# Kernel tuning notes

Hardware: AMD Instinct MI355X
Metric: run time of the kernel (lower is better)

The kernel has to match this reference:

```python
import jax, jax.numpy as jnp
import numpy as np

K = 5            # srn kernel size (kernels[0])
EPSILON = 1e-3   # epsilons -> SRN additive noise scale
BN_EPS = 1e-5
NUM_SLICES = 3
OUT_CH = 64
CLASSES = 5


def _unfold(x, k):
    # torch.nn.Unfold, padding=0: (B, C*k*k, L), channel-major then (kh, kw) row-major
    B, C, H, W = x.shape
    Ho, Wo = H - k + 1, W - k + 1
    cols = jnp.stack([x[:, :, i:i + Ho, j:j + Wo]
                      for i in range(k) for j in range(k)], axis=2)  # (B,C,k*k,Ho,Wo)
    return cols.reshape(B, C * k * k, Ho * Wo), Ho, Wo


def _bn(x, g, b):
    # BatchNorm2d in training mode: batch statistics, biased variance
    m = x.mean((0, 2, 3), keepdims=True)
    v = x.var((0, 2, 3), keepdims=True)
    return (x - m) * jax.lax.rsqrt(v + BN_EPS) * g[None, :, None, None] + b[None, :, None, None]


def _conv(x, w, b):
    y = jax.lax.conv_general_dilated(x, w, (1, 1), 'VALID',
                                     dimension_numbers=('NCHW', 'OIHW', 'NCHW'))
    return y + b[None, :, None, None]


def _avgpool(x, s):
    B, C, H, W = x.shape
    return x.reshape(B, C, H // s, s, W // s, s).mean((3, 5))


def _maxpool(x, s):
    B, C, H, W = x.shape
    return x.reshape(B, C, H // s, s, W // s, s).max((3, 5))


def _srn(x, srn_w):
    B = x.shape[0]
    y, Ho, Wo = _unfold(x, K)                               # (B, n, L)
    y = y + EPSILON * jax.random.normal(jax.random.key(42), y.shape, y.dtype)
    gg = jnp.std(y, axis=1, ddof=1, keepdims=True)          # torch.std is unbiased
    y = y / gg
    O, C, _, _, S = srn_w.shape
    n = C * K * K
    X = srn_w.reshape(O, n, S)
    X = jnp.concatenate([jnp.ones((O, n, 1), X.dtype), X], axis=2)   # (O, n, S+1)
    Xcov = jnp.einsum('onf,ong->ofg', X, X)                 # X^T X, (O, 4, 4)
    Xinv = jnp.linalg.inv(Xcov)
    M = jnp.einsum('ofg,ong->ofn', Xinv, X)
    Wc = jnp.einsum('ofn,bnl->bofl', M, y)
    pred = jnp.einsum('onf,bofl->bonl', X, Wc)              # fitted values (B,O,n,L)
    err = jnp.mean((y[:, None] - pred) ** 2, axis=2)        # (B,O,L)
    err = err.reshape(B, O, Ho, Wo)
    A = (jnp.exp(-err) - np.exp(-1.0)) / (1.0 - np.exp(-1.0))
    return A - 0.5


def setup_inputs() -> dict:
    key = jax.random.key(0)
    ks = jax.random.split(key, 12)
    x = jax.random.normal(ks[0], (4, 3, 64, 64), jnp.float32)
    # xavier-style init scaled up for numerical stability of the small-matrix inverse
    srn_w = 0.05 * jax.random.normal(ks[1], (OUT_CH, 3, K, K, NUM_SLICES), jnp.float32)
    conv2_w = 0.05 * jax.random.normal(ks[2], (128, 64, 3, 3), jnp.float32)
    conv2_b = 0.01 * jax.random.normal(ks[3], (128,), jnp.float32)
    conv3_w = 0.05 * jax.random.normal(ks[4], (128, 128, 3, 3), jnp.float32)
    conv3_b = 0.01 * jax.random.normal(ks[5], (128,), jnp.float32)
    conv4_w = 0.05 * jax.random.normal(ks[6], (128, 128, 3, 3), jnp.float32)
    conv4_b = 0.01 * jax.random.normal(ks[7], (128,), jnp.float32)
    bn1_g = jnp.ones((64,), jnp.float32); bn1_b = jnp.zeros((64,), jnp.float32)
    bn2_g = jnp.ones((128,), jnp.float32); bn2_b = jnp.zeros((128,), jnp.float32)
    bn3_g = jnp.ones((128,), jnp.float32); bn3_b = jnp.zeros((128,), jnp.float32)
    bn4_g = jnp.ones((128,), jnp.float32); bn4_b = jnp.zeros((128,), jnp.float32)
    fc2_w = 0.05 * jax.random.normal(ks[8], (CLASSES, 128, 1, 1), jnp.float32)
    fc2_b = 0.01 * jax.random.normal(ks[9], (CLASSES,), jnp.float32)
    return dict(x=x, srn_w=srn_w, conv2_w=conv2_w, conv2_b=conv2_b,
                conv3_w=conv3_w, conv3_b=conv3_b, conv4_w=conv4_w, conv4_b=conv4_b,
                bn1_g=bn1_g, bn1_b=bn1_b, bn2_g=bn2_g, bn2_b=bn2_b,
                bn3_g=bn3_g, bn3_b=bn3_b, bn4_g=bn4_g, bn4_b=bn4_b,
                fc2_w=fc2_w, fc2_b=fc2_b)


def reference(x, srn_w, conv2_w, conv2_b, conv3_w, conv3_b, conv4_w, conv4_b,
              bn1_g, bn1_b, bn2_g, bn2_b, bn3_g, bn3_b, bn4_g, bn4_b,
              fc2_w, fc2_b):
    h = _srn(x, srn_w)                                      # (B,64,60,60)
    h = _avgpool(h, 2)
    h = _bn(h, bn1_g, bn1_b)
    h = jax.nn.relu(_bn(_conv(h, conv2_w, conv2_b), bn2_g, bn2_b))
    h = _avgpool(h, 2)
    h = jax.nn.relu(_bn(_conv(h, conv3_w, conv3_b), bn3_g, bn3_b))
    h = _maxpool(h, 2)
    h = jax.nn.relu(_bn(_conv(h, conv4_w, conv4_b), bn4_g, bn4_b))
    h = _maxpool(h, 4)                                      # (B,128,1,1)
    flat = h.reshape(h.shape[0], -1)                        # (B,128)
    return flat @ fc2_w.reshape(CLASSES, -1).T + fc2_b      # 1x1 conv == matmul
```

## Files before the change

### kernel.cpp

```cpp
#include <hip/hip_runtime.h>
#include <math.h>

__device__ __align__(16) float g_w2p[9 * 2304 * 4];
__device__ __align__(16) float g_w3p[17 * 2304 * 4];
__device__ __align__(16) float g_w4p[8 * 4608 * 4];
__device__ __align__(16) float g_h1[4 * 30 * 30 * 64];
__device__ __align__(16) float g_h2[4 * 14 * 14 * 4 * 128];
__device__ __align__(16) float g_h3[4 * 6 * 6 * 4 * 128];
__device__ __align__(16) float g_h4[4 * 16 * 128];

__global__ __launch_bounds__(256) void k_srn(const float* __restrict__ x,
                                             const float* __restrict__ srn_w,
                                             const float* __restrict__ w2,
                                             float* __restrict__ stats) {
    __shared__ __align__(16) float wlds[64 * 244];
    __shared__ float xsm[648];
    __shared__ float part[2 * 15 * 66];
    __shared__ float redS[256], redQ[256];
    int bid = blockIdx.x, t = threadIdx.x;
    int b = bid / 60, rem = bid % 60, r = rem >> 1, ch = rem & 1;

    for (int j = bid * 256 + t; j < 73728; j += 240 * 256) {
        int c = j & 3, s4 = j >> 2;
        int sl = s4 % 36, tmp = s4 / 36, oc_l = tmp & 63, blk = tmp >> 6;
        int it = blk & 3, ocg = blk >> 2;
        int kw = sl % 3, icq = (sl / 3) & 3, kh = sl / 12;
        int ic = it * 16 + icq * 4 + c;
        g_w2p[j] = w2[((ocg * 64 + oc_l) * 64 + ic) * 9 + kh * 3 + kw];
    }

    float4 wr[15];
#pragma unroll
    for (int k = 0; k < 15; k++) {
        int i4 = k * 256 + t;
        if (i4 < 3600) wr[k] = ((const float4*)srn_w)[i4];
    }
    float xr[3];
#pragma unroll
    for (int k = 0; k < 3; k++) {
        int i = t + k * 256;
        if (i < 648) {
            int c = i / 216, rm = i % 216, rr = rm / 36, col = rm % 36;
            int gc = ch * 30 + col; if (gc > 63) gc = 63;
            xr[k] = x[((b * 3 + c) * 64 + (2 * r + rr)) * 64 + gc];
        }
    }
#pragma unroll
    for (int k = 0; k < 15; k++) {
        int i4 = k * 256 + t;
        if (i4 < 3600) {
            float v[4] = { wr[k].x, wr[k].y, wr[k].z, wr[k].w };
#pragma unroll
            for (int e = 0; e < 4; e++) {
                int i = i4 * 4 + e, o = i / 225, j = i % 225;
                wlds[o * 244 + (j / 15) * 16 + (j % 15)] = v[e];
            }
        }
    }
#pragma unroll
    for (int k = 0; k < 3; k++) { int i = t + k * 256; if (i < 648) xsm[i] = xr[k]; }
    __syncthreads();

    int w = t >> 6, o = t & 63;
    int rw = w & 1, cq = w >> 1, base = cq * 16;

    float z1[16], z2[16], z3[16], s[16], q[16];
#pragma unroll
    for (int i = 0; i < 16; i++) { z1[i]=0; z2[i]=0; z3[i]=0; s[i]=0; q[i]=0; }

    for (int c = 0; c < 3; c++) {
#pragma unroll
        for (int kh = 0; kh < 5; kh++) {
            float xv[20];
#pragma unroll
            for (int k = 0; k < 20; k++) xv[k] = xsm[(c * 6 + rw + kh) * 36 + base + k];
            float wf[16];
            const float* wp = &wlds[o * 244 + (c * 5 + kh) * 16];
            *(float4*)&wf[0]  = *(const float4*)&wp[0];
            *(float4*)&wf[4]  = *(const float4*)&wp[4];
            *(float4*)&wf[8]  = *(const float4*)&wp[8];
            *(float4*)&wf[12] = *(const float4*)&wp[12];
#pragma unroll
            for (int kw = 0; kw < 5; kw++) {
                float w1 = wf[kw * 3], w2v = wf[kw * 3 + 1], w3v = wf[kw * 3 + 2];
#pragma unroll
                for (int i = 0; i < 16; i++) {
                    float v = xv[kw + i];
                    s[i] += v; q[i] += v * v;
                    z1[i] += w1 * v; z2[i] += w2v * v; z3[i] += w3v * v;
                }
            }
        }
    }

    float gm[16];
    {
        float c01=0,c02=0,c03=0,c11=0,c12=0,c13=0,c22=0,c23=0,c33=0;
#pragma unroll
        for (int row = 0; row < 15; row++) {
            float wf[16];
            const float* wp = &wlds[o * 244 + row * 16];
            *(float4*)&wf[0]  = *(const float4*)&wp[0];
            *(float4*)&wf[4]  = *(const float4*)&wp[4];
            *(float4*)&wf[8]  = *(const float4*)&wp[8];
            *(float4*)&wf[12] = *(const float4*)&wp[12];
#pragma unroll
            for (int kw = 0; kw < 5; kw++) {
                float w1 = wf[kw*3], w2v = wf[kw*3+1], w3v = wf[kw*3+2];
                c01 += w1; c02 += w2v; c03 += w3v;
                c11 += w1*w1; c12 += w1*w2v; c13 += w1*w3v;
                c22 += w2v*w2v; c23 += w2v*w3v; c33 += w3v*w3v;
            }
        }
        float A[4][8];
        A[0][0]=75.f; A[0][1]=c01; A[0][2]=c02; A[0][3]=c03;
        A[1][0]=c01;  A[1][1]=c11; A[1][2]=c12; A[1][3]=c13;
        A[2][0]=c02;  A[2][1]=c12; A[2][2]=c22; A[2][3]=c23;
        A[3][0]=c03;  A[3][1]=c13; A[3][2]=c23; A[3][3]=c33;
#pragma unroll
        for (int i = 0; i < 4; i++)
#pragma unroll
            for (int j = 0; j < 4; j++) A[i][4 + j] = (i == j) ? 1.f : 0.f;
#pragma unroll
        for (int p = 0; p < 4; p++) {
            float ip = 1.f / A[p][p];
#pragma unroll
            for (int j = 0; j < 8; j++) A[p][j] *= ip;
#pragma unroll
            for (int i = 0; i < 4; i++) if (i != p) {
                float f = A[i][p];
#pragma unroll
                for (int j = 0; j < 8; j++) A[i][j] -= f * A[p][j];
            }
        }
#pragma unroll
        for (int i = 0; i < 4; i++)
#pragma unroll
            for (int j = 0; j < 4; j++) gm[i * 4 + j] = A[i][4 + j];
    }

    const float C1 = 0.36787944117144233f;
    const float INV = 1.5819767068693265f;
#pragma unroll
    for (int pp = 0; pp < 8; pp++) {
        int pl = cq * 8 + pp;
        if (pl < 15) {
            float aa = 0.f;
#pragma unroll
            for (int e = 0; e < 2; e++) {
                int i = 2 * pp + e;
                float sum = s[i], sq = q[i];
                float gg2 = (sq - sum * sum * (1.f / 75.f)) * (1.f / 74.f);
                float zf[4] = { sum, z1[i], z2[i], z3[i] };
                float qf = 0.f;
#pragma unroll
                for (int f = 0; f < 4; f++) {
                    float acc = 0.f;
#pragma unroll
                    for (int h = 0; h < 4; h++) acc += gm[f * 4 + h] * zf[h];
                    qf += acc * zf[f];
                }
                float err = (sq - qf) / (75.f * gg2);
                aa += (expf(-err) - C1) * INV - 0.5f;
            }
            part[(rw * 15 + pl) * 66 + o] = 0.25f * aa;
        }
    }
    __syncthreads();

    int j = t >> 6;
    float ps = 0.f, pq = 0.f;
    for (int pl = j; pl < 15; pl += 4) {
        float v = part[pl * 66 + o] + part[(15 + pl) * 66 + o];
        g_h1[((b * 30 + r) * 30 + ch * 15 + pl) * 64 + o] = v;
        ps += v; pq += v * v;
    }
    redS[t] = ps; redQ[t] = pq;
    __syncthreads();
    if (t < 64) {
        atomicAdd(&stats[t],      redS[t] + redS[64 + t] + redS[128 + t] + redS[192 + t]);
        atomicAdd(&stats[64 + t], redQ[t] + redQ[64 + t] + redQ[128 + t] + redQ[192 + t]);
    }
}

__global__ __launch_bounds__(256) void k_conv2(const float* __restrict__ w3,
                                               const float* __restrict__ g1,
                                               const float* __restrict__ b1,
                                               float* __restrict__ stats) {
    __shared__ __align__(16) float ws[64 * 148];
    __shared__ __align__(16) float xs[3 * 30 * 64];
    __shared__ float redS[256], redQ[256];
    int blk = blockIdx.x;
    int b = blk / 56, rem = blk % 56, oh = rem >> 1, ocg = rem & 1;
    int t = threadIdx.x;
    int oc_l = t & 63, qtr = t >> 6, owb = qtr * 7;

    for (int j = blk * 256 + t; j < 147456; j += 224 * 256) {
        int c = j & 3, s4 = j >> 2;
        int sl = s4 % 36, tmp = s4 / 36, oc2 = tmp & 63, bk = tmp >> 6;
        int it = bk & 7, og = bk >> 3;
        int kw = sl % 3, icq = (sl / 3) & 3, kh = sl / 12;
        int ic = it * 16 + icq * 4 + c;
        g_w3p[j] = w3[((og * 64 + oc2) * 128 + ic) * 9 + kh * 3 + kw];
    }

    {
        int icb = (t & 15) * 4;
        float4 S = *(const float4*)&stats[icb], Q = *(const float4*)&stats[64 + icb];
        float4 G4 = *(const float4*)&g1[icb], B4 = *(const float4*)&b1[icb];
        float scv[4], shv[4];
        float mm[4] = { S.x, S.y, S.z, S.w }, qq[4] = { Q.x, Q.y, Q.z, Q.w };
        float gg[4] = { G4.x, G4.y, G4.z, G4.w }, bb[4] = { B4.x, B4.y, B4.z, B4.w };
#pragma unroll
        for (int c = 0; c < 4; c++) {
            float m = mm[c] * (1.f / 3600.f);
            float v = qq[c] * (1.f / 3600.f) - m * m;
            scv[c] = gg[c] * rsqrtf(v + 1e-5f);
            shv[c] = bb[c] - m * scv[c];
        }
        const float4* src4 = (const float4*)(g_h1 + (b * 900 + oh * 30) * 64);
        float4 xr[6];
#pragma unroll
        for (int k = 0; k < 6; k++) { int i4 = t + k * 256; if (i4 < 1440) xr[k] = src4[i4]; }
        const float4* wsrc0 = (const float4*)g_w2p;
        float4 wreg[9];
#pragma unroll
        for (int k = 0; k < 9; k++) wreg[k] = wsrc0[(ocg * 4) * 2304 + k * 256 + t];
#pragma unroll
        for (int k = 0; k < 6; k++) {
            int i4 = t + k * 256;
            if (i4 < 1440) {
                float4 v;
                v.x = xr[k].x * scv[0] + shv[0]; v.y = xr[k].y * scv[1] + shv[1];
                v.z = xr[k].z * scv[2] + shv[2]; v.w = xr[k].w * scv[3] + shv[3];
                *(float4*)&xs[i4 * 4] = v;
            }
        }
#pragma unroll
        for (int k = 0; k < 9; k++) {
            int idx = k * 256 + t;
            *(float4*)&ws[(idx / 36) * 148 + (idx % 36) * 4] = wreg[k];
        }
    }
    __syncthreads();

    float acc[7] = {0, 0, 0, 0, 0, 0, 0};
    const float4* wsrc = (const float4*)g_w2p + (ocg * 4) * 2304;
    for (int it = 0; it < 4; ++it) {
        float4 wreg[9];
        if (it < 3) {
#pragma unroll
            for (int k = 0; k < 9; k++) wreg[k] = wsrc[(it + 1) * 2304 + k * 256 + t];
        }
#pragma unroll 1
        for (int icq = 0; icq < 4; icq++) {
            int xoff = it * 16 + icq * 4;
#pragma unroll
            for (int kh = 0; kh < 3; kh++) {
                const float* wb = &ws[oc_l * 148 + (kh * 4 + icq) * 12];
                float4 w0 = *(const float4*)&wb[0];
                float4 w1 = *(const float4*)&wb[4];
                float4 w2v = *(const float4*)&wb[8];
                const float* xrow = &xs[(kh * 30 + owb) * 64 + xoff];
                float4 x0 = *(const float4*)&xrow[0];
                float4 x1 = *(const float4*)&xrow[64];
#pragma unroll
                for (int i = 0; i < 7; i++) {
                    float4 x2 = *(const float4*)&xrow[(i + 2) * 64];
                    acc[i] += w0.x * x0.x + w0.y * x0.y + w0.z * x0.z + w0.w * x0.w
                            + w1.x * x1.x + w1.y * x1.y + w1.z * x1.z + w1.w * x1.w
                            + w2v.x * x2.x + w2v.y * x2.y + w2v.z * x2.z + w2v.w * x2.w;
                    x0 = x1; x1 = x2;
                }
            }
        }
        if (it < 3) {
            __syncthreads();
#pragma unroll
            for (int k = 0; k < 9; k++) {
                int idx = k * 256 + t;
                *(float4*)&ws[(idx / 36) * 148 + (idx % 36) * 4] = wreg[k];
            }
            __syncthreads();
        }
    }
    int oc = ocg * 64 + oc_l;
    float ps = 0.f, pq = 0.f;
#pragma unroll
    for (int i = 0; i < 7; i++) {
        int ow = owb + i;
        g_h2[(((b * 14 + (oh >> 1)) * 14 + (ow >> 1)) * 4 + (oh & 1) * 2 + (ow & 1)) * 128 + oc] = acc[i];
        ps += acc[i]; pq += acc[i] * acc[i];
    }
    redS[t] = ps; redQ[t] = pq;
    __syncthreads();
    if (t < 64) {
        atomicAdd(&stats[128 + ocg * 64 + t], redS[t] + redS[64 + t] + redS[128 + t] + redS[192 + t]);
        atomicAdd(&stats[256 + ocg * 64 + t], redQ[t] + redQ[64 + t] + redQ[128 + t] + redQ[192 + t]);
    }
}

__global__ __launch_bounds__(256) void k_conv3(const float* __restrict__ w4,
                                               const float* __restrict__ g2,
                                               const float* __restrict__ b2,
                                               float* __restrict__ stats) {
    __shared__ __align__(16) float ws[64 * 148];
    __shared__ __align__(16) float xs[3 * 14 * 128];
    __shared__ float redS[256], redQ[256];
    int blk = blockIdx.x;
    int b = blk / 24, rem = blk % 24, oh = rem >> 1, ocg = rem & 1;
    int t = threadIdx.x;
    int oc_l = t & 63, qtr = t >> 6, owb = qtr * 3;

    for (int j = blk * 256 + t; j < 147456; j += 96 * 256) {
        int c = j & 3, s4 = j >> 2;
        int sl = s4 % 72, tmp = s4 / 72, oc2 = tmp & 15, blkq = tmp >> 4;
        int icq = blkq & 3, og = blkq >> 2;
        int kw = sl % 3, icb2 = (sl / 3) & 7, kh = sl / 24;
        int ic = icq * 32 + icb2 * 4 + c;
        g_w4p[j] = w4[((og * 16 + oc2) * 128 + ic) * 9 + kh * 3 + kw];
    }

    {
        int icb = (t & 31) * 4;
        float4 S = *(const float4*)&stats[128 + icb], Q = *(const float4*)&stats[256 + icb];
        float4 G4 = *(const float4*)&g2[icb], B4 = *(const float4*)&b2[icb];
        float scv[4], shv[4];
        float mm[4] = { S.x, S.y, S.z, S.w }, qq[4] = { Q.x, Q.y, Q.z, Q.w };
        float gg[4] = { G4.x, G4.y, G4.z, G4.w }, bb[4] = { B4.x, B4.y, B4.z, B4.w };
#pragma unroll
        for (int c = 0; c < 4; c++) {
            float m = mm[c] * (1.f / 3136.f);
            float v = qq[c] * (1.f / 3136.f) - m * m;
            scv[c] = gg[c] * rsqrtf(v + 1e-5f);
            shv[c] = bb[c] - m * scv[c];
        }
        const float4* wsrc0 = (const float4*)g_w3p;
        float4 wreg[9];
#pragma unroll
        for (int k = 0; k < 9; k++) wreg[k] = wsrc0[(ocg * 8) * 2304 + k * 256 + t];
        float4 pa[6], pb[6], pc[6], pd[6];
#pragma unroll
        for (int k = 0; k < 6; k++) {
            int i4 = t + k * 256;
            if (i4 < 1344) {
                int px = (i4 >> 5) % 14, rr = i4 / 448;
                const float4* p0 = (const float4*)&g_h2[(((b * 14 + oh + rr) * 14 + px) * 4) * 128 + (i4 & 31) * 4];
                pa[k] = p0[0]; pb[k] = p0[32]; pc[k] = p0[64]; pd[k] = p0[96];
            }
        }
#pragma unroll
        for (int k = 0; k < 9; k++) {
            int idx = k * 256 + t;
            *(float4*)&ws[(idx / 36) * 148 + (idx % 36) * 4] = wreg[k];
        }
#pragma unroll
        for (int k = 0; k < 6; k++) {
            int i4 = t + k * 256;
            if (i4 < 1344) {
                float4 o4;
                o4.x = 0.25f * (fmaxf(pa[k].x * scv[0] + shv[0], 0.f) + fmaxf(pb[k].x * scv[0] + shv[0], 0.f)
                              + fmaxf(pc[k].x * scv[0] + shv[0], 0.f) + fmaxf(pd[k].x * scv[0] + shv[0], 0.f));
                o4.y = 0.25f * (fmaxf(pa[k].y * scv[1] + shv[1], 0.f) + fmaxf(pb[k].y * scv[1] + shv[1], 0.f)
                              + fmaxf(pc[k].y * scv[1] + shv[1], 0.f) + fmaxf(pd[k].y * scv[1] + shv[1], 0.f));
                o4.z = 0.25f * (fmaxf(pa[k].z * scv[2] + shv[2], 0.f) + fmaxf(pb[k].z * scv[2] + shv[2], 0.f)
                              + fmaxf(pc[k].z * scv[2] + shv[2], 0.f) + fmaxf(pd[k].z * scv[2] + shv[2], 0.f));
                o4.w = 0.25f * (fmaxf(pa[k].w * scv[3] + shv[3], 0.f) + fmaxf(pb[k].w * scv[3] + shv[3], 0.f)
                              + fmaxf(pc[k].w * scv[3] + shv[3], 0.f) + fmaxf(pd[k].w * scv[3] + shv[3], 0.f));
                *(float4*)&xs[i4 * 4] = o4;
            }
        }
    }
    __syncthreads();

    float acc[3] = {0, 0, 0};
    const float4* wsrc = (const float4*)g_w3p + (ocg * 8) * 2304;
    for (int it = 0; it < 8; ++it) {
        float4 wreg[9];
        if (it < 7) {
#pragma unroll
            for (int k = 0; k < 9; k++) wreg[k] = wsrc[(it + 1) * 2304 + k * 256 + t];
        }
#pragma unroll 1
        for (int icq = 0; icq < 4; icq++) {
            int xoff = it * 16 + icq * 4;
#pragma unroll
            for (int kh = 0; kh < 3; kh++) {
                const float* wb = &ws[oc_l * 148 + (kh * 4 + icq) * 12];
                float4 w0 = *(const float4*)&wb[0];
                float4 w1 = *(const float4*)&wb[4];
                float4 w2v = *(const float4*)&wb[8];
                const float* xrow = &xs[(kh * 14 + owb) * 128 + xoff];
                float4 x0 = *(const float4*)&xrow[0];
                float4 x1 = *(const float4*)&xrow[128];
#pragma unroll
                for (int i = 0; i < 3; i++) {
                    float4 x2 = *(const float4*)&xrow[(i + 2) * 128];
                    acc[i] += w0.x * x0.x + w0.y * x0.y + w0.z * x0.z + w0.w * x0.w
                            + w1.x * x1.x + w1.y * x1.y + w1.z * x1.z + w1.w * x1.w
                            + w2v.x * x2.x + w2v.y * x2.y + w2v.z * x2.z + w2v.w * x2.w;
                    x0 = x1; x1 = x2;
                }
            }
        }
        if (it < 7) {
            __syncthreads();
#pragma unroll
            for (int k = 0; k < 9; k++) {
                int idx = k * 256 + t;
                *(float4*)&ws[(idx / 36) * 148 + (idx % 36) * 4] = wreg[k];
            }
            __syncthreads();
        }
    }
    int oc = ocg * 64 + oc_l;
    float ps = 0.f, pq = 0.f;
#pragma unroll
    for (int i = 0; i < 3; i++) {
        int ow = owb + i;
        g_h3[(((b * 6 + (oh >> 1)) * 6 + (ow >> 1)) * 4 + (oh & 1) * 2 + (ow & 1)) * 128 + oc] = acc[i];
        ps += acc[i]; pq += acc[i] * acc[i];
    }
    redS[t] = ps; redQ[t] = pq;
    __syncthreads();
    if (t < 64) {
        atomicAdd(&stats[384 + ocg * 64 + t], redS[t] + redS[64 + t] + redS[128 + t] + redS[192 + t]);
        atomicAdd(&stats[512 + ocg * 64 + t], redQ[t] + redQ[64 + t] + redQ[128 + t] + redQ[192 + t]);
    }
}

__global__ __launch_bounds__(256) void k_conv4(const float* __restrict__ g3,
                                               const float* __restrict__ b3,
                                               float* __restrict__ stats) {
    __shared__ __align__(16) float ws[64 * 292];
    __shared__ __align__(16) float xs[3 * 6 * 128];
    __shared__ float red[256];
    int blk = blockIdx.x;
    int b = blk / 32, rem = blk % 32, oh = rem / 8, ocg = rem % 8;
    int t = threadIdx.x;
    int oc_l = t & 15, ow = (t >> 4) & 3, icq = t >> 6;

    {
        int icb = (t & 31) * 4;
        float4 S = *(const float4*)&stats[384 + icb], Q = *(const float4*)&stats[512 + icb];
        float4 G4 = *(const float4*)&g3[icb], B4 = *(const float4*)&b3[icb];
        float scv[4], shv[4];
        float mm[4] = { S.x, S.y, S.z, S.w }, qq[4] = { Q.x, Q.y, Q.z, Q.w };
        float gg[4] = { G4.x, G4.y, G4.z, G4.w }, bb[4] = { B4.x, B4.y, B4.z, B4.w };
#pragma unroll
        for (int c = 0; c < 4; c++) {
            float m = mm[c] * (1.f / 576.f);
            float v = qq[c] * (1.f / 576.f) - m * m;
            scv[c] = gg[c] * rsqrtf(v + 1e-5f);
            shv[c] = bb[c] - m * scv[c];
        }
        const float4* wsrc = (const float4*)g_w4p + ocg * 4608;
        float4 wreg[18];
#pragma unroll
        for (int k = 0; k < 18; k++) wreg[k] = wsrc[k * 256 + t];
        float4 pa[3], pb[3], pc[3], pd[3];
#pragma unroll
        for (int k = 0; k < 3; k++) {
            int i4 = t + k * 256;
            if (i4 < 576) {
                int px = (i4 >> 5) % 6, rr = i4 / 192;
                const float4* p0 = (const float4*)&g_h3[(((b * 6 + oh + rr) * 6 + px) * 4) * 128 + (i4 & 31) * 4];
                pa[k] = p0[0]; pb[k] = p0[32]; pc[k] = p0[64]; pd[k] = p0[96];
            }
        }
#pragma unroll
        for (int k = 0; k < 18; k++) {
            int idx = k * 256 + t;
            *(float4*)&ws[(idx / 72) * 292 + (idx % 72) * 4] = wreg[k];
        }
#pragma unroll
        for (int k = 0; k < 3; k++) {
            int i4 = t + k * 256;
            if (i4 < 576) {
                float4 o4;
                o4.x = fmaxf(fmaxf(fmaxf(pa[k].x * scv[0] + shv[0], pb[k].x * scv[0] + shv[0]),
                                   fmaxf(pc[k].x * scv[0] + shv[0], pd[k].x * scv[0] + shv[0])), 0.f);
                o4.y = fmaxf(fmaxf(fmaxf(pa[k].y * scv[1] + shv[1], pb[k].y * scv[1] + shv[1]),
                                   fmaxf(pc[k].y * scv[1] + shv[1], pd[k].y * scv[1] + shv[1])), 0.f);
                o4.z = fmaxf(fmaxf(fmaxf(pa[k].z * scv[2] + shv[2], pb[k].z * scv[2] + shv[2]),
                                   fmaxf(pc[k].z * scv[2] + shv[2], pd[k].z * scv[2] + shv[2])), 0.f);
                o4.w = fmaxf(fmaxf(fmaxf(pa[k].w * scv[3] + shv[3], pb[k].w * scv[3] + shv[3]),
                                   fmaxf(pc[k].w * scv[3] + shv[3], pd[k].w * scv[3] + shv[3])), 0.f);
                *(float4*)&xs[i4 * 4] = o4;
            }
        }
    }
    __syncthreads();

    float acc = 0.f;
    const float* wbase = &ws[(icq * 16 + oc_l) * 292];
#pragma unroll 1
    for (int icbq = 0; icbq < 8; icbq++) {
#pragma unroll
        for (int kh = 0; kh < 3; kh++) {
            const float* wb = &wbase[(kh * 8 + icbq) * 12];
            float4 w0 = *(const float4*)&wb[0];
            float4 w1 = *(const float4*)&wb[4];
            float4 w2v = *(const float4*)&wb[8];
            float4 x0 = *(const float4*)&xs[(kh * 6 + ow) * 128 + icq * 32 + icbq * 4];
            float4 x1 = *(const float4*)&xs[(kh * 6 + ow + 1) * 128 + icq * 32 + icbq * 4];
            float4 x2 = *(const float4*)&xs[(kh * 6 + ow + 2) * 128 + icq * 32 + icbq * 4];
            acc += w0.x * x0.x + w0.y * x0.y + w0.z * x0.z + w0.w * x0.w
                 + w1.x * x1.x + w1.y * x1.y + w1.z * x1.z + w1.w * x1.w
                 + w2v.x * x2.x + w2v.y * x2.y + w2v.z * x2.z + w2v.w * x2.w;
        }
    }
    red[t] = acc;
    __syncthreads();
    if (t < 64) {
        float v = red[t] + red[t + 64] + red[t + 128] + red[t + 192];
        int oc = ocg * 16 + (t & 15);
        g_h4[((b * 4 + oh) * 4 + (t >> 4)) * 128 + oc] = v;
        float ps = v + __shfl_xor(v, 16);  ps += __shfl_xor(ps, 32);
        float pv = v * v;
        float pq = pv + __shfl_xor(pv, 16); pq += __shfl_xor(pq, 32);
        if (t < 16) {
            atomicAdd(&stats[640 + ocg * 16 + t], ps);
            atomicAdd(&stats[768 + ocg * 16 + t], pq);
        }
    }
}

__global__ __launch_bounds__(256) void k_final(const float* __restrict__ g4,
                                               const float* __restrict__ b4,
                                               const float* __restrict__ fcw,
                                               const float* __restrict__ fcb,
                                               const float* __restrict__ stats,
                                               float* __restrict__ out) {
    __shared__ float sc[128], sh[128];
    __shared__ float pooled[4][128];
    int t = threadIdx.x;
    if (t < 128) {
        float m = stats[640 + t] * (1.f / 64.f);
        float v = stats[768 + t] * (1.f / 64.f) - m * m;
        float rs = rsqrtf(v + 1e-5f);
        sc[t] = g4[t] * rs; sh[t] = b4[t] - m * sc[t];
    }
    __syncthreads();
    for (int item = t; item < 512; item += 256) {
        int b = item >> 7, oc = item & 127;
        float s = sc[oc], h = sh[oc];
        float mx = 0.f;
#pragma unroll
        for (int k = 0; k < 16; k++) mx = fmaxf(mx, g_h4[(b * 16 + k) * 128 + oc] * s + h);
        pooled[b][oc] = mx;
    }
    __syncthreads();
    if (t < 20) {
        int b = t / 5, cls = t % 5;
        float acc = fcb[cls];
        const float* w = &fcw[cls * 128];
        for (int oc = 0; oc < 128; oc++) acc += pooled[b][oc] * w[oc];
        out[b * 5 + cls] = acc;
    }
}

extern "C" void kernel_launch(void* const* d_in, const int* in_sizes, int n_in,
                              void* d_out, int out_size, void* d_ws, size_t ws_size,
                              hipStream_t stream) {
    (void)in_sizes; (void)n_in; (void)out_size; (void)ws_size;
    const float* x     = (const float*)d_in[0];
    const float* srn_w = (const float*)d_in[1];
    const float* w2    = (const float*)d_in[2];
    const float* w3    = (const float*)d_in[4];
    const float* w4    = (const float*)d_in[6];
    const float* g1 = (const float*)d_in[8];  const float* b1 = (const float*)d_in[9];
    const float* g2 = (const float*)d_in[10]; const float* b2 = (const float*)d_in[11];
    const float* g3 = (const float*)d_in[12]; const float* b3 = (const float*)d_in[13];
    const float* g4 = (const float*)d_in[14]; const float* b4 = (const float*)d_in[15];
    const float* fcw = (const float*)d_in[16]; const float* fcb = (const float*)d_in[17];
    float* out = (float*)d_out;
    float* stats = (float*)d_ws;

    hipMemsetAsync(d_ws, 0, 4096, stream);
    k_srn  <<<dim3(240), dim3(256), 0, stream>>>(x, srn_w, w2, stats);
    k_conv2<<<dim3(224), dim3(256), 0, stream>>>(w3, g1, b1, stats);
    k_conv3<<<dim3(96),  dim3(256), 0, stream>>>(w4, g2, b2, stats);
    k_conv4<<<dim3(128), dim3(256), 0, stream>>>(g3, b3, stats);
    k_final<<<dim3(1),   dim3(256), 0, stream>>>(g4, b4, fcw, fcb, stats, out);
}
```

Baseline: 111.2 us.

## Double parallelism in SRN/conv kernels and replace stat atomics with per-block partials

Result: slower. 144.6 us (+30.1%).

```diff
diff --git a/kernel.cpp b/kernel.cpp
--- a/kernel.cpp
+++ b/kernel.cpp
@@ -1,44 +1,53 @@
 #include <hip/hip_runtime.h>
 #include <math.h>
 
-__device__ __align__(16) float g_w2p[9 * 2304 * 4];
-__device__ __align__(16) float g_w3p[17 * 2304 * 4];
+#define P1S 0
+#define P1Q 15360
+#define P2S 30720
+#define P2Q 45056
+#define P3S 59392
+#define P3Q 65536
+#define P4S 71680
+#define P4Q 73728
+
+__device__ __align__(16) float g_w2p[16 * 1152 * 4];
+__device__ __align__(16) float g_w3p[32 * 1152 * 4];
 __device__ __align__(16) float g_w4p[8 * 4608 * 4];
 __device__ __align__(16) float g_h1[4 * 30 * 30 * 64];
 __device__ __align__(16) float g_h2[4 * 14 * 14 * 4 * 128];
 __device__ __align__(16) float g_h3[4 * 6 * 6 * 4 * 128];
 __device__ __align__(16) float g_h4[4 * 16 * 128];
 
-__global__ __launch_bounds__(256) void k_srn(const float* __restrict__ x,
+__global__ __launch_bounds__(512) void k_srn(const float* __restrict__ x,
                                              const float* __restrict__ srn_w,
                                              const float* __restrict__ w2,
-                                             float* __restrict__ stats) {
+                                             float* __restrict__ ws) {
     __shared__ __align__(16) float wlds[64 * 244];
     __shared__ float xsm[648];
     __shared__ float part[2 * 15 * 66];
-    __shared__ float redS[256], redQ[256];
+    __shared__ float redS[512], redQ[512];
     int bid = blockIdx.x, t = threadIdx.x;
     int b = bid / 60, rem = bid % 60, r = rem >> 1, ch = rem & 1;
 
-    for (int j = bid * 256 + t; j < 73728; j += 240 * 256) {
+    for (int j = bid * 512 + t; j < 73728; j += 240 * 512) {
         int c = j & 3, s4 = j >> 2;
-        int sl = s4 % 36, tmp = s4 / 36, oc_l = tmp & 63, blk = tmp >> 6;
+        int sl = s4 % 36, tmp = s4 / 36, oc_l = tmp & 31, blk = tmp >> 5;
         int it = blk & 3, ocg = blk >> 2;
         int kw = sl % 3, icq = (sl / 3) & 3, kh = sl / 12;
         int ic = it * 16 + icq * 4 + c;
-        g_w2p[j] = w2[((ocg * 64 + oc_l) * 64 + ic) * 9 + kh * 3 + kw];
-    }
-
-    float4 wr[15];
-#pragma unroll
-    for (int k = 0; k < 15; k++) {
-        int i4 = k * 256 + t;
+        g_w2p[j] = w2[((ocg * 32 + oc_l) * 64 + ic) * 9 + kh * 3 + kw];
+    }
+
+    float4 wr[8];
+#pragma unroll
+    for (int k = 0; k < 8; k++) {
+        int i4 = k * 512 + t;
         if (i4 < 3600) wr[k] = ((const float4*)srn_w)[i4];
     }
-    float xr[3];
-#pragma unroll
-    for (int k = 0; k < 3; k++) {
-        int i = t + k * 256;
+    float xr[2];
+#pragma unroll
+    for (int k = 0; k < 2; k++) {
+        int i = k * 512 + t;
         if (i < 648) {
             int c = i / 216, rm = i % 216, rr = rm / 36, col = rm % 36;
             int gc = ch * 30 + col; if (gc > 63) gc = 63;
@@ -46,34 +55,34 @@
         }
     }
 #pragma unroll
-    for (int k = 0; k < 15; k++) {
-        int i4 = k * 256 + t;
+    for (int k = 0; k < 8; k++) {
+        int i4 = k * 512 + t;
         if (i4 < 3600) {
-            float v[4] = { wr[k].x, wr[k].y, wr[k].z, wr[k].w };
+            float v4[4] = { wr[k].x, wr[k].y, wr[k].z, wr[k].w };
 #pragma unroll
             for (int e = 0; e < 4; e++) {
-                int i = i4 * 4 + e, o = i / 225, j = i % 225;
-                wlds[o * 244 + (j / 15) * 16 + (j % 15)] = v[e];
-            }
-        }
-    }
-#pragma unroll
-    for (int k = 0; k < 3; k++) { int i = t + k * 256; if (i < 648) xsm[i] = xr[k]; }
+                int i = i4 * 4 + e, o = i / 225, jj = i % 225;
+                wlds[o * 244 + (jj / 15) * 16 + (jj % 15)] = v4[e];
+            }
+        }
+    }
+#pragma unroll
+    for (int k = 0; k < 2; k++) { int i = k * 512 + t; if (i < 648) xsm[i] = xr[k]; }
     __syncthreads();
 
     int w = t >> 6, o = t & 63;
-    int rw = w & 1, cq = w >> 1, base = cq * 16;
-
-    float z1[16], z2[16], z3[16], s[16], q[16];
-#pragma unroll
-    for (int i = 0; i < 16; i++) { z1[i]=0; z2[i]=0; z3[i]=0; s[i]=0; q[i]=0; }
+    int rw = w & 1, cq = w >> 1, base = cq * 8;
+
+    float z1[8], z2[8], z3[8], s[8], q[8];
+#pragma unroll
+    for (int i = 0; i < 8; i++) { z1[i]=0; z2[i]=0; z3[i]=0; s[i]=0; q[i]=0; }
 
     for (int c = 0; c < 3; c++) {
 #pragma unroll
         for (int kh = 0; kh < 5; kh++) {
-            float xv[20];
-#pragma unroll
-            for (int k = 0; k < 20; k++) xv[k] = xsm[(c * 6 + rw + kh) * 36 + base + k];
+            float xv[12];
+#pragma unroll
+            for (int k = 0; k < 12; k++) xv[k] = xsm[(c * 6 + rw + kh) * 36 + base + k];
             float wf[16];
             const float* wp = &wlds[o * 244 + (c * 5 + kh) * 16];
             *(float4*)&wf[0]  = *(const float4*)&wp[0];
@@ -84,7 +93,7 @@
             for (int kw = 0; kw < 5; kw++) {
                 float w1 = wf[kw * 3], w2v = wf[kw * 3 + 1], w3v = wf[kw * 3 + 2];
 #pragma unroll
-                for (int i = 0; i < 16; i++) {
+                for (int i = 0; i < 8; i++) {
                     float v = xv[kw + i];
                     s[i] += v; q[i] += v * v;
                     z1[i] += w1 * v; z2[i] += w2v * v; z3[i] += w3v * v;
@@ -142,8 +151,8 @@
     const float C1 = 0.36787944117144233f;
     const float INV = 1.5819767068693265f;
 #pragma unroll
-    for (int pp = 0; pp < 8; pp++) {
-        int pl = cq * 8 + pp;
+    for (int pp = 0; pp < 4; pp++) {
+        int pl = cq * 4 + pp;
         if (pl < 15) {
             float aa = 0.f;
 #pragma unroll
@@ -168,9 +177,9 @@
     }
     __syncthreads();
 
-    int j = t >> 6;
+    int j2 = t >> 6;
     float ps = 0.f, pq = 0.f;
-    for (int pl = j; pl < 15; pl += 4) {
+    for (int pl = j2; pl < 15; pl += 8) {
         float v = part[pl * 66 + o] + part[(15 + pl) * 66 + o];
         g_h1[((b * 30 + r) * 30 + ch * 15 + pl) * 64 + o] = v;
         ps += v; pq += v * v;
@@ -178,54 +187,67 @@
     redS[t] = ps; redQ[t] = pq;
     __syncthreads();
     if (t < 64) {
-        atomicAdd(&stats[t],      redS[t] + redS[64 + t] + redS[128 + t] + redS[192 + t]);
-        atomicAdd(&stats[64 + t], redQ[t] + redQ[64 + t] + redQ[128 + t] + redQ[192 + t]);
+        float aS = 0.f, aQ = 0.f;
+#pragma unroll
+        for (int k = 0; k < 8; k++) { aS += redS[t + 64 * k]; aQ += redQ[t + 64 * k]; }
+        ws[P1S + bid * 64 + t] = aS;
+        ws[P1Q + bid * 64 + t] = aQ;
     }
 }
 
 __global__ __launch_bounds__(256) void k_conv2(const float* __restrict__ w3,
                                                const float* __restrict__ g1,
                                                const float* __restrict__ b1,
-                                               float* __restrict__ stats) {
-    __shared__ __align__(16) float ws[64 * 148];
+                                               float* __restrict__ ws) {
+    __shared__ __align__(16) float wsl[32 * 148];
     __shared__ __align__(16) float xs[3 * 30 * 64];
     __shared__ float redS[256], redQ[256];
-    int blk = blockIdx.x;
-    int b = blk / 56, rem = blk % 56, oh = rem >> 1, ocg = rem & 1;
-    int t = threadIdx.x;
-    int oc_l = t & 63, qtr = t >> 6, owb = qtr * 7;
-
-    for (int j = blk * 256 + t; j < 147456; j += 224 * 256) {
+    __shared__ float sc1[64], sh1[64];
+    int blk = blockIdx.x, t = threadIdx.x;
+    int b = blk / 112, rem = blk % 112, oh = rem >> 2, ocg = rem & 3;
+    int oc_l = t & 31, grp = t >> 5;
+    int now = (grp < 4) ? 4 : 3;
+    int owb = (grp < 4) ? grp * 4 : 16 + (grp - 4) * 3;
+
+    for (int j = blk * 256 + t; j < 147456; j += 448 * 256) {
         int c = j & 3, s4 = j >> 2;
-        int sl = s4 % 36, tmp = s4 / 36, oc2 = tmp & 63, bk = tmp >> 6;
+        int sl = s4 % 36, tmp = s4 / 36, ocl = tmp & 31, bk = tmp >> 5;
         int it = bk & 7, og = bk >> 3;
         int kw = sl % 3, icq = (sl / 3) & 3, kh = sl / 12;
         int ic = it * 16 + icq * 4 + c;
-        g_w3p[j] = w3[((og * 64 + oc2) * 128 + ic) * 9 + kh * 3 + kw];
+        g_w3p[j] = w3[((og * 32 + ocl) * 128 + ic) * 9 + kh * 3 + kw];
+    }
+
+    {
+        int chh = t & 63, jj = t >> 6;
+        float aS = 0.f, aQ = 0.f;
+        for (int i = jj; i < 240; i += 4) { aS += ws[P1S + i * 64 + chh]; aQ += ws[P1Q + i * 64 + chh]; }
+        redS[t] = aS; redQ[t] = aQ;
+        __syncthreads();
+        if (t < 64) {
+            float S = redS[t] + redS[64 + t] + redS[128 + t] + redS[192 + t];
+            float Q = redQ[t] + redQ[64 + t] + redQ[128 + t] + redQ[192 + t];
+            float m = S * (1.f / 3600.f);
+            float v = Q * (1.f / 3600.f) - m * m;
+            float scv = g1[t] * rsqrtf(v + 1e-5f);
+            sc1[t] = scv; sh1[t] = b1[t] - m * scv;
+        }
+        __syncthreads();
     }
 
     {
         int icb = (t & 15) * 4;
-        float4 S = *(const float4*)&stats[icb], Q = *(const float4*)&stats[64 + icb];
-        float4 G4 = *(const float4*)&g1[icb], B4 = *(const float4*)&b1[icb];
         float scv[4], shv[4];
-        float mm[4] = { S.x, S.y, S.z, S.w }, qq[4] = { Q.x, Q.y, Q.z, Q.w };
-        float gg[4] = { G4.x, G4.y, G4.z, G4.w }, bb[4] = { B4.x, B4.y, B4.z, B4.w };
-#pragma unroll
-        for (int c = 0; c < 4; c++) {
-            float m = mm[c] * (1.f / 3600.f);
-            float v = qq[c] * (1.f / 3600.f) - m * m;
-            scv[c] = gg[c] * rsqrtf(v + 1e-5f);
-            shv[c] = bb[c] - m * scv[c];
-        }
+#pragma unroll
+        for (int c = 0; c < 4; c++) { scv[c] = sc1[icb + c]; shv[c] = sh1[icb + c]; }
         const float4* src4 = (const float4*)(g_h1 + (b * 900 + oh * 30) * 64);
         float4 xr[6];
 #pragma unroll
         for (int k = 0; k < 6; k++) { int i4 = t + k * 256; if (i4 < 1440) xr[k] = src4[i4]; }
-        const float4* wsrc0 = (const float4*)g_w2p;
-        float4 wreg[9];
-#pragma unroll
-        for (int k = 0; k < 9; k++) wreg[k] = wsrc0[(ocg * 4) * 2304 + k * 256 + t];
+        const float4* wsrc0 = (const float4*)g_w2p + (ocg * 4) * 1152;
+        float4 wreg[5];
+#pragma unroll
+        for (int k = 0; k < 5; k++) { int i4 = k * 256 + t; if (i4 < 1152) wreg[k] = wsrc0[i4]; }
 #pragma unroll
         for (int k = 0; k < 6; k++) {
             int i4 = t + k * 256;
@@ -237,27 +259,27 @@
             }
         }
 #pragma unroll
-        for (int k = 0; k < 9; k++) {
-            int idx = k * 256 + t;
-            *(float4*)&ws[(idx / 36) * 148 + (idx % 36) * 4] = wreg[k];
-        }
-    }
-    __syncthreads();
-
-    float acc[7] = {0, 0, 0, 0, 0, 0, 0};
-    const float4* wsrc = (const float4*)g_w2p + (ocg * 4) * 2304;
+        for (int k = 0; k < 5; k++) {
+            int i4 = k * 256 + t;
+            if (i4 < 1152) *(float4*)&wsl[(i4 / 36) * 148 + (i4 % 36) * 4] = wreg[k];
+        }
+    }
+    __syncthreads();
+
+    float acc[4] = {0, 0, 0, 0};
+    const float4* wsrc = (const float4*)g_w2p + (ocg * 4) * 1152;
     for (int it = 0; it < 4; ++it) {
-        float4 wreg[9];
+        float4 wreg[5];
         if (it < 3) {
 #pragma unroll
-            for (int k = 0; k < 9; k++) wreg[k] = wsrc[(it + 1) * 2304 + k * 256 + t];
+            for (int k = 0; k < 5; k++) { int i4 = k * 256 + t; if (i4 < 1152) wreg[k] = wsrc[(it + 1) * 1152 + i4]; }
         }
 #pragma unroll 1
         for (int icq = 0; icq < 4; icq++) {
             int xoff = it * 16 + icq * 4;
 #pragma unroll
             for (int kh = 0; kh < 3; kh++) {
-                const float* wb = &ws[oc_l * 148 + (kh * 4 + icq) * 12];
+                const float* wb = &wsl[oc_l * 148 + (kh * 4 + icq) * 12];
                 float4 w0 = *(const float4*)&wb[0];
                 float4 w1 = *(const float4*)&wb[4];
                 float4 w2v = *(const float4*)&wb[8];
@@ -265,54 +287,63 @@
                 float4 x0 = *(const float4*)&xrow[0];
                 float4 x1 = *(const float4*)&xrow[64];
 #pragma unroll
-                for (int i = 0; i < 7; i++) {
-                    float4 x2 = *(const float4*)&xrow[(i + 2) * 64];
-                    acc[i] += w0.x * x0.x + w0.y * x0.y + w0.z * x0.z + w0.w * x0.w
-                            + w1.x * x1.x + w1.y * x1.y + w1.z * x1.z + w1.w * x1.w
-                            + w2v.x * x2.x + w2v.y * x2.y + w2v.z * x2.z + w2v.w * x2.w;
-                    x0 = x1; x1 = x2;
+                for (int i = 0; i < 4; i++) {
+                    if (i < now) {
+                        float4 x2 = *(const float4*)&xrow[(i + 2) * 64];
+                        acc[i] += w0.x * x0.x + w0.y * x0.y + w0.z * x0.z + w0.w * x0.w
+                                + w1.x * x1.x + w1.y * x1.y + w1.z * x1.z + w1.w * x1.w
+                                + w2v.x * x2.x + w2v.y * x2.y + w2v.z * x2.z + w2v.w * x2.w;
+                        x0 = x1; x1 = x2;
+                    }
                 }
             }
         }
         if (it < 3) {
             __syncthreads();
 #pragma unroll
-            for (int k = 0; k < 9; k++) {
-                int idx = k * 256 + t;
-                *(float4*)&ws[(idx / 36) * 148 + (idx % 36) * 4] = wreg[k];
+            for (int k = 0; k < 5; k++) {
+                int i4 = k * 256 + t;
+                if (i4 < 1152) *(float4*)&wsl[(i4 / 36) * 148 + (i4 % 36) * 4] = wreg[k];
             }
             __syncthreads();
         }
     }
-    int oc = ocg * 64 + oc_l;
+    int oc = ocg * 32 + oc_l;
     float ps = 0.f, pq = 0.f;
 #pragma unroll
-    for (int i = 0; i < 7; i++) {
-        int ow = owb + i;
-        g_h2[(((b * 14 + (oh >> 1)) * 14 + (ow >> 1)) * 4 + (oh & 1) * 2 + (ow & 1)) * 128 + oc] = acc[i];
-        ps += acc[i]; pq += acc[i] * acc[i];
+    for (int i = 0; i < 4; i++) {
+        if (i < now) {
+            int ow = owb + i;
+            g_h2[(((b * 14 + (oh >> 1)) * 14 + (ow >> 1)) * 4 + (oh & 1) * 2 + (ow & 1)) * 128 + oc] = acc[i];
+            ps += acc[i]; pq += acc[i] * acc[i];
+        }
     }
     redS[t] = ps; redQ[t] = pq;
     __syncthreads();
-    if (t < 64) {
-        atomicAdd(&stats[128 + ocg * 64 + t], redS[t] + redS[64 + t] + redS[128 + t] + redS[192 + t]);
-        atomicAdd(&stats[256 + ocg * 64 + t], redQ[t] + redQ[64 + t] + redQ[128 + t] + redQ[192 + t]);
+    if (t < 32) {
+        float aS = 0.f, aQ = 0.f;
+#pragma unroll
+        for (int k = 0; k < 8; k++) { aS += redS[t + 32 * k]; aQ += redQ[t + 32 * k]; }
+        ws[P2S + blk * 32 + t] = aS;
+        ws[P2Q + blk * 32 + t] = aQ;
     }
 }
 
 __global__ __launch_bounds__(256) void k_conv3(const float* __restrict__ w4,
                                                const float* __restrict__ g2,
                                                const float* __restrict__ b2,
-                                               float* __restrict__ stats) {
-    __shared__ __align__(16) float ws[64 * 148];
+                                               float* __restrict__ ws) {
+    __shared__ __align__(16) float wsl[32 * 148];
     __shared__ __align__(16) float xs[3 * 14 * 128];
     __shared__ float redS[256], redQ[256];
-    int blk = blockIdx.x;
-    int b = blk / 24, rem = blk % 24, oh = rem >> 1, ocg = rem & 1;
-    int t = threadIdx.x;
-    int oc_l = t & 63, qtr = t >> 6, owb = qtr * 3;
-
-    for (int j = blk * 256 + t; j < 147456; j += 96 * 256) {
+    __shared__ float sc2[128], sh2[128];
+    int blk = blockIdx.x, t = threadIdx.x;
+    int b = blk / 48, rem = blk % 48, oh = rem >> 2, ocg = rem & 3;
+    int oc_l = t & 31, grp = t >> 5;
+    int now = (grp < 4) ? 2 : 1;
+    int owb = (grp < 4) ? grp * 2 : 8 + (grp - 4);
+
+    for (int j = blk * 256 + t; j < 147456; j += 192 * 256) {
         int c = j & 3, s4 = j >> 2;
         int sl = s4 % 72, tmp = s4 / 72, oc2 = tmp & 15, blkq = tmp >> 4;
         int icq = blkq & 3, og = blkq >> 2;
@@ -322,23 +353,34 @@
     }
 
     {
+        int chh = t & 127, jj = t >> 7;
+        float aS = 0.f, aQ = 0.f;
+        for (int i = jj; i < 112; i += 2) {
+            int idx = (i * 4 + (chh >> 5)) * 32 + (chh & 31);
+            aS += ws[P2S + idx]; aQ += ws[P2Q + idx];
+        }
+        redS[t] = aS; redQ[t] = aQ;
+        __syncthreads();
+        if (t < 128) {
+            float S = redS[t] + redS[128 + t];
+            float Q = redQ[t] + redQ[128 + t];
+            float m = S * (1.f / 3136.f);
+            float v = Q * (1.f / 3136.f) - m * m;
+            float scv = g2[t] * rsqrtf(v + 1e-5f);
+            sc2[t] = scv; sh2[t] = b2[t] - m * scv;
+        }
+        __syncthreads();
+    }
+
+    {
         int icb = (t & 31) * 4;
-        float4 S = *(const float4*)&stats[128 + icb], Q = *(const float4*)&stats[256 + icb];
-        float4 G4 = *(const float4*)&g2[icb], B4 = *(const float4*)&b2[icb];
         float scv[4], shv[4];
-        float mm[4] = { S.x, S.y, S.z, S.w }, qq[4] = { Q.x, Q.y, Q.z, Q.w };
-        float gg[4] = { G4.x, G4.y, G4.z, G4.w }, bb[4] = { B4.x, B4.y, B4.z, B4.w };
-#pragma unroll
-        for (int c = 0; c < 4; c++) {
-            float m = mm[c] * (1.f / 3136.f);
-            float v = qq[c] * (1.f / 3136.f) - m * m;
-            scv[c] = gg[c] * rsqrtf(v + 1e-5f);
-            shv[c] = bb[c] - m * scv[c];
-        }
-        const float4* wsrc0 = (const float4*)g_w3p;
-        float4 wreg[9];
-#pragma unroll
-        for (int k = 0; k < 9; k++) wreg[k] = wsrc0[(ocg * 8) * 2304 + k * 256 + t];
+#pragma unroll
+        for (int c = 0; c < 4; c++) { scv[c] = sc2[icb + c]; shv[c] = sh2[icb + c]; }
+        const float4* wsrc0 = (const float4*)g_w3p + (ocg * 8) * 1152;
+        float4 wreg[5];
+#pragma unroll
+        for (int k = 0; k < 5; k++) { int i4 = k * 256 + t; if (i4 < 1152) wreg[k] = wsrc0[i4]; }
         float4 pa[6], pb[6], pc[6], pd[6];
 #pragma unroll
         for (int k = 0; k < 6; k++) {
@@ -350,9 +392,9 @@
             }
         }
 #pragma unroll
-        for (int k = 0; k < 9; k++) {
-            int idx = k * 256 + t;
-            *(float4*)&ws[(idx / 36) * 148 + (idx % 36) * 4] = wreg[k];
+        for (int k = 0; k < 5; k++) {
+            int i4 = k * 256 + t;
+            if (i4 < 1152) *(float4*)&wsl[(i4 / 36) * 148 + (i4 % 36) * 4] = wreg[k];
         }
 #pragma unroll
         for (int k = 0; k < 6; k++) {
@@ -373,20 +415,20 @@
     }
     __syncthreads();
 
-    float acc[3] = {0, 0, 0};
-    const float4* wsrc = (const float4*)g_w3p + (ocg * 8) * 2304;
+    float acc[2] = {0, 0};
+    const float4* wsrc = (const float4*)g_w3p + (ocg * 8) * 1152;
     for (int it = 0; it < 8; ++it) {
-        float4 wreg[9];
+        float4 wreg[5];
         if (it < 7) {
 #pragma unroll
-            for (int k = 0; k < 9; k++) wreg[k] = wsrc[(it + 1) * 2304 + k * 256 + t];
+            for (int k = 0; k < 5; k++) { int i4 = k * 256 + t; if (i4 < 1152) wreg[k] = wsrc[(it + 1) * 1152 + i4]; }
         }
 #pragma unroll 1
         for (int icq = 0; icq < 4; icq++) {
             int xoff = it * 16 + icq * 4;
 #pragma unroll
             for (int kh = 0; kh < 3; kh++) {
-                const float* wb = &ws[oc_l * 148 + (kh * 4 + icq) * 12];
+                const float* wb = &wsl[oc_l * 148 + (kh * 4 + icq) * 12];
                 float4 w0 = *(const float4*)&wb[0];
                 float4 w1 = *(const float4*)&wb[4];
                 float4 w2v = *(const float4*)&wb[8];
@@ -394,66 +436,84 @@
                 float4 x0 = *(const float4*)&xrow[0];
                 float4 x1 = *(const float4*)&xrow[128];
 #pragma unroll
-                for (int i = 0; i < 3; i++) {
-                    float4 x2 = *(const float4*)&xrow[(i + 2) * 128];
-                    acc[i] += w0.x * x0.x + w0.y * x0.y + w0.z * x0.z + w0.w * x0.w
-                            + w1.x * x1.x + w1.y * x1.y + w1.z * x1.z + w1.w * x1.w
-                            + w2v.x * x2.x + w2v.y * x2.y + w2v.z * x2.z + w2v.w * x2.w;
-                    x0 = x1; x1 = x2;
+                for (int i = 0; i < 2; i++) {
+                    if (i < now) {
+                        float4 x2 = *(const float4*)&xrow[(i + 2) * 128];
+                        acc[i] += w0.x * x0.x + w0.y * x0.y + w0.z * x0.z + w0.w * x0.w
+                                + w1.x * x1.x + w1.y * x1.y + w1.z * x1.z + w1.w * x1.w
+                                + w2v.x * x2.x + w2v.y * x2.y + w2v.z * x2.z + w2v.w * x2.w;
+                        x0 = x1; x1 = x2;
+                    }
                 }
             }
         }
         if (it < 7) {
             __syncthreads();
 #pragma unroll
-            for (int k = 0; k < 9; k++) {
-                int idx = k * 256 + t;
-                *(float4*)&ws[(idx / 36) * 148 + (idx % 36) * 4] = wreg[k];
+            for (int k = 0; k < 5; k++) {
+                int i4 = k * 256 + t;
+                if (i4 < 1152) *(float4*)&wsl[(i4 / 36) * 148 + (i4 % 36) * 4] = wreg[k];
             }
             __syncthreads();
         }
     }
-    int oc = ocg * 64 + oc_l;
+    int oc = ocg * 32 + oc_l;
     float ps = 0.f, pq = 0.f;
 #pragma unroll
-    for (int i = 0; i < 3; i++) {
-        int ow = owb + i;
-        g_h3[(((b * 6 + (oh >> 1)) * 6 + (ow >> 1)) * 4 + (oh & 1) * 2 + (ow & 1)) * 128 + oc] = acc[i];
-        ps += acc[i]; pq += acc[i] * acc[i];
+    for (int i = 0; i < 2; i++) {
+        if (i < now) {
+            int ow = owb + i;
+            g_h3[(((b * 6 + (oh >> 1)) * 6 + (ow >> 1)) * 4 + (oh & 1) * 2 + (ow & 1)) * 128 + oc] = acc[i];
+            ps += acc[i]; pq += acc[i] * acc[i];
+        }
     }
     redS[t] = ps; redQ[t] = pq;
     __syncthreads();
-    if (t < 64) {
-        atomicAdd(&stats[384 + ocg * 64 + t], redS[t] + redS[64 + t] + redS[128 + t] + redS[192 + t]);
-        atomicAdd(&stats[512 + ocg * 64 + t], redQ[t] + redQ[64 + t] + redQ[128 + t] + redQ[192 + t]);
+    if (t < 32) {
+        float aS = 0.f, aQ = 0.f;
+#pragma unroll
+        for (int k = 0; k < 8; k++) { aS += redS[t + 32 * k]; aQ += redQ[t + 32 * k]; }
+        ws[P3S + blk * 32 + t] = aS;
+        ws[P3Q + blk * 32 + t] = aQ;
     }
 }
 
 __global__ __launch_bounds__(256) void k_conv4(const float* __restrict__ g3,
                                                const float* __restrict__ b3,
-                                               float* __restrict__ stats) {
-    __shared__ __align__(16) float ws[64 * 292];
+                                               float* __restrict__ ws) {
+    __shared__ __align__(16) float wsl[64 * 292];
     __shared__ __align__(16) float xs[3 * 6 * 128];
-    __shared__ float red[256];
-    int blk = blockIdx.x;
+    __shared__ float red[256], redQ2[256];
+    __shared__ float sc3[128], sh3[128];
+    int blk = blockIdx.x, t = threadIdx.x;
     int b = blk / 32, rem = blk % 32, oh = rem / 8, ocg = rem % 8;
-    int t = threadIdx.x;
     int oc_l = t & 15, ow = (t >> 4) & 3, icq = t >> 6;
+
+    {
+        int chh = t & 127, jj = t >> 7;
+        float aS = 0.f, aQ = 0.f;
+        for (int i = jj; i < 48; i += 2) {
+            int idx = (i * 4 + (chh >> 5)) * 32 + (chh & 31);
+            aS += ws[P3S + idx]; aQ += ws[P3Q + idx];
+        }
+        red[t] = aS; redQ2[t] = aQ;
+        __syncthreads();
+        if (t < 128) {
+            float S = red[t] + red[128 + t];
+            float Q = redQ2[t] + redQ2[128 + t];
+            float m = S * (1.f / 576.f);
+            float v = Q * (1.f / 576.f) - m * m;
+            float scv = g3[t] * rsqrtf(v + 1e-5f);
+            sc3[t] = scv; sh3[t] = b3[t] - m * scv;
+        }
+        __syncthreads();
+    }
 
     {
         int icb = (t & 31) * 4;
-        float4 S = *(const float4*)&stats[384 + icb], Q = *(const float4*)&stats[512 + icb];
-        float4 G4 = *(const float4*)&g3[icb], B4 = *(const float4*)&b3[icb];
         float scv[4], shv[4];
-        float mm[4] = { S.x, S.y, S.z, S.w }, qq[4] = { Q.x, Q.y, Q.z, Q.w };
-        float gg[4] = { G4.x, G4.y, G4.z, G4.w }, bb[4] = { B4.x, B4.y, B4.z, B4.w };
-#pragma unroll
-        for (int c = 0; c < 4; c++) {
-            float m = mm[c] * (1.f / 576.f);
-            float v = qq[c] * (1.f / 576.f) - m * m;
-            scv[c] = gg[c] * rsqrtf(v + 1e-5f);
-            shv[c] = bb[c] - m * scv[c];
-        }
+#pragma unroll
+        for (int c = 0; c < 4; c++) { scv[c] = sc3[icb + c]; shv[c] = sh3[icb + c]; }
         const float4* wsrc = (const float4*)g_w4p + ocg * 4608;
         float4 wreg[18];
 #pragma unroll
@@ -471,7 +531,7 @@
 #pragma unroll
         for (int k = 0; k < 18; k++) {
             int idx = k * 256 + t;
-            *(float4*)&ws[(idx / 72) * 292 + (idx % 72) * 4] = wreg[k];
+            *(float4*)&wsl[(idx / 72) * 292 + (idx % 72) * 4] = wreg[k];
         }
 #pragma unroll
         for (int k = 0; k < 3; k++) {
@@ -493,7 +553,7 @@
     __syncthreads();
 
     float acc = 0.f;
-    const float* wbase = &ws[(icq * 16 + oc_l) * 292];
+    const float* wbase = &wsl[(icq * 16 + oc_l) * 292];
 #pragma unroll 1
     for (int icbq = 0; icbq < 8; icbq++) {
 #pragma unroll
@@ -520,8 +580,8 @@
         float pv = v * v;
         float pq = pv + __shfl_xor(pv, 16); pq += __shfl_xor(pq, 32);
         if (t < 16) {
-            atomicAdd(&stats[640 + ocg * 16 + t], ps);
-            atomicAdd(&stats[768 + ocg * 16 + t], pq);
+            ws[P4S + blk * 16 + t] = ps;
+            ws[P4Q + blk * 16 + t] = pq;
         }
     }
 }
@@ -530,33 +590,39 @@
                                                const float* __restrict__ b4,
                                                const float* __restrict__ fcw,
                                                const float* __restrict__ fcb,
-                                               const float* __restrict__ stats,
+                                               const float* __restrict__ ws,
                                                float* __restrict__ out) {
     __shared__ float sc[128], sh[128];
     __shared__ float pooled[4][128];
     int t = threadIdx.x;
     if (t < 128) {
-        float m = stats[640 + t] * (1.f / 64.f);
-        float v = stats[768 + t] * (1.f / 64.f) - m * m;
+        float S = 0.f, Q = 0.f;
+#pragma unroll
+        for (int i = 0; i < 16; i++) {
+            int idx = (i * 8 + (t >> 4)) * 16 + (t & 15);
+            S += ws[P4S + idx]; Q += ws[P4Q + idx];
+        }
+        float m = S * (1.f / 64.f);
+        float v = Q * (1.f / 64.f) - m * m;
         float rs = rsqrtf(v + 1e-5f);
         sc[t] = g4[t] * rs; sh[t] = b4[t] - m * sc[t];
     }
     __syncthreads();
     for (int item = t; item < 512; item += 256) {
-        int b = item >> 7, oc = item & 127;
+        int bb = item >> 7, oc = item & 127;
         float s = sc[oc], h = sh[oc];
         float mx = 0.f;
 #pragma unroll
-        for (int k = 0; k < 16; k++) mx = fmaxf(mx, g_h4[(b * 16 + k) * 128 + oc] * s + h);
-        pooled[b][oc] = mx;
+        for (int k = 0; k < 16; k++) mx = fmaxf(mx, g_h4[(bb * 16 + k) * 128 + oc] * s + h);
+        pooled[bb][oc] = mx;
     }
     __syncthreads();
     if (t < 20) {
-        int b = t / 5, cls = t % 5;
+        int bb = t / 5, cls = t % 5;
         float acc = fcb[cls];
         const float* w = &fcw[cls * 128];
-        for (int oc = 0; oc < 128; oc++) acc += pooled[b][oc] * w[oc];
-        out[b * 5 + cls] = acc;
+        for (int oc = 0; oc < 128; oc++) acc += pooled[bb][oc] * w[oc];
+        out[bb * 5 + cls] = acc;
     }
 }
 
@@ -575,12 +641,11 @@
     const float* g4 = (const float*)d_in[14]; const float* b4 = (const float*)d_in[15];
     const float* fcw = (const float*)d_in[16]; const float* fcb = (const float*)d_in[17];
     float* out = (float*)d_out;
-    float* stats = (float*)d_ws;
-
-    hipMemsetAsync(d_ws, 0, 4096, stream);
-    k_srn  <<<dim3(240), dim3(256), 0, stream>>>(x, srn_w, w2, stats);
-    k_conv2<<<dim3(224), dim3(256), 0, stream>>>(w3, g1, b1, stats);
-    k_conv3<<<dim3(96),  dim3(256), 0, stream>>>(w4, g2, b2, stats);
-    k_conv4<<<dim3(128), dim3(256), 0, stream>>>(g3, b3, stats);
-    k_final<<<dim3(1),   dim3(256), 0, stream>>>(g4, b4, fcw, fcb, stats, out);
+    float* ws = (float*)d_ws;
+
+    k_srn  <<<dim3(240), dim3(512), 0, stream>>>(x, srn_w, w2, ws);
+    k_conv2<<<dim3(448), dim3(256), 0, stream>>>(w3, g1, b1, ws);
+    k_conv3<<<dim3(192), dim3(256), 0, stream>>>(w4, g2, b2, ws);
+    k_conv4<<<dim3(128), dim3(256), 0, stream>>>(g3, b3, ws);
+    k_final<<<dim3(1),   dim3(256), 0, stream>>>(g4, b4, fcw, fcb, ws, out);
 }
```
